# Kernel optimization log

Hardware: AMD Instinct MI355X
Metric: run time of the kernel (lower is better)

## Reference

```python
import math
import jax, jax.numpy as jnp
import numpy as np

D_MODEL = 1024
NUM_HEADS = 16
D_K = D_MODEL // NUM_HEADS
THETA = 10000.0
MAX_SEQ_LEN = 2048
BATCH = 2
SEQ = 2048


def build_rope_matrices(theta, d_k, max_seq_len):
    # Faithful to the torch buffer: per-position d_k x d_k tridiagonal rotation matrix.
    k = jnp.arange(d_k)
    inv_freq = jnp.power(theta, -2.0 * (k // 2) / d_k)  # [d_k]
    pos = jnp.arange(max_seq_len, dtype=jnp.float32)[:, None]  # [S,1]
    ang = pos * inv_freq[None, :]  # [S, d_k]
    cos_v = jnp.cos(ang)  # main diagonal
    sin_v = jnp.sin(jnp.where(k % 2 == 0, ang, 0.0))[:, :-1]  # sub/super diagonal, len d_k-1

    def mk(c, s):
        return jnp.diag(c) + jnp.diag(s, -1) + jnp.diag(-s, 1)

    return jax.vmap(mk)(cos_v, sin_v)  # [max_seq_len, d_k, d_k]


def setup_inputs() -> dict:
    key = jax.random.key(0)
    k1, k2, k3 = jax.random.split(key, 3)
    x = jax.random.normal(k1, (BATCH, SEQ, D_MODEL), dtype=jnp.float32)
    token_positions = jnp.arange(SEQ, dtype=jnp.int64 if jax.config.jax_enable_x64 else jnp.int32)
    # trunc_normal init approximated by scaled normal (same distribution family / scale)
    std_attn = 2.0 / (D_MODEL + 3 * D_MODEL)
    std_out = 2.0 / (D_MODEL + D_MODEL)
    W_attn = jax.random.normal(k2, (3 * NUM_HEADS * D_K, D_MODEL), dtype=jnp.float32) * std_attn
    W_out = jax.random.normal(k3, (D_MODEL, NUM_HEADS * D_K), dtype=jnp.float32) * std_out
    rope = build_rope_matrices(THETA, D_K, MAX_SEQ_LEN)
    return {"x": x, "W_attn": W_attn, "W_out": W_out, "rope": rope,
            "token_positions": token_positions}


def reference(x, W_attn, W_out, rope, token_positions):
    B, S, _ = x.shape
    # QKV projection: '... d_in, d_out d_in -> ... d_out'
    proj = jnp.einsum('bsd,ed->bse', x, W_attn)  # [B,S,3*H*dk]
    proj = proj.reshape(B, S, 3, NUM_HEADS, D_K)
    proj = jnp.transpose(proj, (2, 0, 3, 1, 4))  # [3,B,H,S,dk]
    Q, K, V = proj[0], proj[1], proj[2]
    # RoPE via per-position matrix multiply (faithful to module)
    R = rope[token_positions]  # [S, dk, dk]
    Q = jnp.einsum('sij,bhsj->bhsi', R, Q)
    K = jnp.einsum('sij,bhsj->bhsi', R, K)
    # naive causal attention with full score matrix (faithful)
    scores = jnp.einsum('bhnd,bhmd->bhnm', Q, K) / math.sqrt(D_K)
    causal = jnp.tril(jnp.ones((S, S), dtype=bool))
    scores = jnp.where(causal, scores, -jnp.inf)
    attn = jax.nn.softmax(scores, axis=-1)
    attended = jnp.einsum('bhnm,bhmd->bhnd', attn, V)  # [B,H,S,dk]
    concat = jnp.transpose(attended, (0, 2, 1, 3)).reshape(B, S, NUM_HEADS * D_K)
    return jnp.einsum('bse,de->bsd', concat, W_out)
```

## Files before the change

### kernel.cpp

```cpp
#include <hip/hip_runtime.h>
#include <math.h>

#define B_SZ 2
#define SEQ 2048
#define DMODEL 1024
#define NH 16
#define DK 64
#define NQKV 3072
#define M_ROWS 4096

#define NEG_BIG (-3.0e38f)
#define SCL 0.18033688011112042f

typedef short short8 __attribute__((ext_vector_type(8)));
typedef float v4f __attribute__((ext_vector_type(4)));
typedef unsigned short ushort_t;

__device__ inline ushort_t f2bf(float f) {
    unsigned u = __float_as_uint(f);
    u += 0x7fffu + ((u >> 16) & 1u);
    return (ushort_t)(u >> 16);
}

__device__ __forceinline__ void gl_lds16(const ushort_t* g, ushort_t* l) {
    __builtin_amdgcn_global_load_lds(
        (const __attribute__((address_space(1))) unsigned int*)g,
        (__attribute__((address_space(3))) unsigned int*)l, 16, 0, 0);
}

__global__ __launch_bounds__(256) void prep_kernel(
    const float* __restrict__ x, const float* __restrict__ Wa,
    const float* __restrict__ Wo, const float* __restrict__ rope,
    ushort_t* __restrict__ xb, ushort_t* __restrict__ Wab, ushort_t* __restrict__ Wob,
    float* __restrict__ cosT, float* __restrict__ sinT)
{
    const int bid = blockIdx.x;
    if (bid < 8192) {
        const float* src; ushort_t* dst; int i;
        if (bid < 4096)      { src = x;  dst = xb;  i = bid * 256 + threadIdx.x; }
        else if (bid < 7168) { src = Wa; dst = Wab; i = (bid - 4096) * 256 + threadIdx.x; }
        else                 { src = Wo; dst = Wob; i = (bid - 7168) * 256 + threadIdx.x; }
        float4 v = reinterpret_cast<const float4*>(src)[i];
        ushort4 r;
        r.x = f2bf(v.x); r.y = f2bf(v.y); r.z = f2bf(v.z); r.w = f2bf(v.w);
        reinterpret_cast<ushort4*>(dst)[i] = r;
    } else {
        const int i = (bid - 8192) * 256 + threadIdx.x;
        const int p = i >> 6, d = i & 63;
        const float* Rp = rope + (size_t)p * 4096;
        const float c = Rp[d * 64 + d];
        const float s = Rp[(d | 1) * 64 + (d & ~1)];
        cosT[i] = c;
        sinT[i] = (d & 1) ? s : -s;
    }
}

#define ES_STRIDE 136
extern __shared__ ushort_t qkv_smem[];

__global__ __launch_bounds__(256) void qkv_mfma_kernel(
    const ushort_t* __restrict__ xb,
    const ushort_t* __restrict__ Wab,
    const float* __restrict__ cosT, const float* __restrict__ sinT,
    const int* __restrict__ tpos,
    ushort_t* __restrict__ Qb, ushort_t* __restrict__ Kb, ushort_t* __restrict__ Vtb)
{
    ushort_t* Es = qkv_smem;

    const int tid = threadIdx.x;
    const int w = tid >> 6, lane = tid & 63;
    const int lm = lane & 15, g = lane >> 4;
    const int wm = (w >> 1) * 64, wn = (w & 1) * 64;
    const int e0 = blockIdx.x * 128, m0 = blockIdx.y * 128;

    int srow[8], skc[8];
#pragma unroll
    for (int j = 0; j < 8; ++j) {
        const int c = tid + 256 * j;
        const int cm = c & 1023;
        const int row = cm >> 3, pp = cm & 7;
        srow[j] = row;
        skc[j] = (pp ^ (row & 7)) * 8;
    }

    v4f acc[4][4] = {};

    for (int k0 = 0; k0 < DMODEL; k0 += 64) {
        __syncthreads();
#pragma unroll
        for (int j = 0; j < 4; ++j)
            gl_lds16(&Wab[(size_t)(e0 + srow[j]) * DMODEL + k0 + skc[j]],
                     &qkv_smem[(tid + 256 * j) * 8]);
#pragma unroll
        for (int j = 4; j < 8; ++j)
            gl_lds16(&xb [(size_t)(m0 + srow[j]) * DMODEL + k0 + skc[j]],
                     &qkv_smem[(tid + 256 * j) * 8]);
        __syncthreads();

#pragma unroll
        for (int kb = 0; kb < 2; ++kb) {
            short8 af[4], bfr[4];
#pragma unroll
            for (int mf = 0; mf < 4; ++mf) {
                const int r = wm + mf * 16 + lm;
                af[mf] = *reinterpret_cast<const short8*>(
                    &qkv_smem[(r * 8 + ((kb * 4 + g) ^ (r & 7))) * 8]);
            }
#pragma unroll
            for (int nf = 0; nf < 4; ++nf) {
                const int r = wn + nf * 16 + lm;
                bfr[nf] = *reinterpret_cast<const short8*>(
                    &qkv_smem[8192 + (r * 8 + ((kb * 4 + g) ^ (r & 7))) * 8]);
            }
#pragma unroll
            for (int mf = 0; mf < 4; ++mf)
#pragma unroll
                for (int nf = 0; nf < 4; ++nf)
                    acc[mf][nf] = __builtin_amdgcn_mfma_f32_16x16x32_bf16(af[mf], bfr[nf], acc[mf][nf], 0, 0, 0);
        }
    }

    __syncthreads();

    const int which = e0 >> 10;
    const int h0 = (e0 & 1023) >> 6;
    const int bb = m0 >> 11, s0 = m0 & 2047;

    if (which < 2) {
        ushort_t* buf = (which == 0) ? Qb : Kb;
#pragma unroll
        for (int mf = 0; mf < 4; ++mf) {
            const int ebase = wm + mf * 16 + g * 4;
            const int d0 = (e0 + ebase) & 63;
#pragma unroll
            for (int nf = 0; nf < 4; ++nf) {
                const int sloc = wn + nf * 16 + lm;
                float v[4] = {acc[mf][nf][0], acc[mf][nf][1], acc[mf][nf][2], acc[mf][nf][3]};
                const int p = tpos[s0 + sloc];
                const float4 c4 = *reinterpret_cast<const float4*>(&cosT[p * 64 + d0]);
                const float4 s4 = *reinterpret_cast<const float4*>(&sinT[p * 64 + d0]);
                const float r0 = c4.x * v[0] + s4.x * v[1];
                const float r1 = c4.y * v[1] + s4.y * v[0];
                const float r2 = c4.z * v[2] + s4.z * v[3];
                const float r3 = c4.w * v[3] + s4.w * v[2];
                uint2 pp;
                pp.x = (unsigned)f2bf(r0) | ((unsigned)f2bf(r1) << 16);
                pp.y = (unsigned)f2bf(r2) | ((unsigned)f2bf(r3) << 16);
                *reinterpret_cast<uint2*>(&Es[sloc * ES_STRIDE + ebase]) = pp;
            }
        }
        __syncthreads();
#pragma unroll
        for (int hh = 0; hh < 2; ++hh) {
            ushort_t* dst = buf + (((size_t)bb * NH + h0 + hh) * SEQ + s0) * DK;
#pragma unroll
            for (int t = 0; t < 4; ++t) {
                const int o = (t * 256 + tid) * 8;
                const int sloc = o >> 6, d = o & 63;
                const short8 vv = *reinterpret_cast<const short8*>(&Es[sloc * ES_STRIDE + hh * 64 + d]);
                *reinterpret_cast<short8*>(&dst[o]) = vv;
            }
        }
    } else {
#pragma unroll
        for (int mf = 0; mf < 4; ++mf) {
            const int ebase = wm + mf * 16 + g * 4;
#pragma unroll
            for (int nf = 0; nf < 4; ++nf) {
                const int sloc = wn + nf * 16 + lm;
                Es[(ebase + 0) * ES_STRIDE + sloc] = f2bf(acc[mf][nf][0]);
                Es[(ebase + 1) * ES_STRIDE + sloc] = f2bf(acc[mf][nf][1]);
                Es[(ebase + 2) * ES_STRIDE + sloc] = f2bf(acc[mf][nf][2]);
                Es[(ebase + 3) * ES_STRIDE + sloc] = f2bf(acc[mf][nf][3]);
            }
        }
        __syncthreads();
#pragma unroll
        for (int t = 0; t < 8; ++t) {
            const int c = t * 256 + tid;
            const int hh = c >> 10, cm = c & 1023;
            const int d = cm >> 4, s8c = (cm & 15) * 8;
            const short8 vv = *reinterpret_cast<const short8*>(&Es[(hh * 64 + d) * ES_STRIDE + s8c]);
            ushort_t* dst = Vtb + ((size_t)bb * NH + h0 + hh) * SEQ * DK + (size_t)d * SEQ + s0 + s8c;
            *reinterpret_cast<short8*>(dst) = vv;
        }
    }
}

#define ATTN_STEP(KSB, VSB, QF0, QF1, QROW, LSUM, OA, DIAG, C0)                   \
    {                                                                             \
        v4f sacc[4] = {};                                                         \
        _Pragma("unroll")                                                         \
        for (int nf = 0; nf < 4; ++nf) {                                          \
            const short8 kf0 = *reinterpret_cast<const short8*>(&KSB[nf * 16 + lm][lk8]);      \
            const short8 kf1 = *reinterpret_cast<const short8*>(&KSB[nf * 16 + lm][32 + lk8]); \
            sacc[nf] = __builtin_amdgcn_mfma_f32_16x16x32_bf16(kf0, QF0, sacc[nf], 0, 0, 0);   \
            sacc[nf] = __builtin_amdgcn_mfma_f32_16x16x32_bf16(kf1, QF1, sacc[nf], 0, 0, 0);   \
        }                                                                         \
        if (DIAG) {                                                               \
            _Pragma("unroll")                                                     \
            for (int nf = 0; nf < 4; ++nf)                                        \
                _Pragma("unroll")                                                 \
                for (int reg = 0; reg < 4; ++reg) {                               \
                    const int kv = (C0) + nf * 16 + g * 4 + reg;                  \
                    const float sv = sacc[nf][reg] * SCL;                         \
                    sacc[nf][reg] = (kv > (QROW)) ? NEG_BIG : sv;                 \
                }                                                                 \
        } else {                                                                  \
            _Pragma("unroll")                                                     \
            for (int nf = 0; nf < 4; ++nf)                                        \
                _Pragma("unroll")                                                 \
                for (int reg = 0; reg < 4; ++reg) sacc[nf][reg] *= SCL;           \
        }                                                                         \
        _Pragma("unroll")                                                         \
        for (int nf = 0; nf < 4; ++nf) {                                          \
            _Pragma("unroll")                                                     \
            for (int reg = 0; reg < 4; ++reg) {                                   \
                const float p = exp2f(sacc[nf][reg]);                             \
                sacc[nf][reg] = p;                                                \
                LSUM += p;                                                        \
            }                                                                     \
            uint2 pp;                                                             \
            pp.x = (unsigned)f2bf(sacc[nf][0]) | ((unsigned)f2bf(sacc[nf][1]) << 16); \
            pp.y = (unsigned)f2bf(sacc[nf][2]) | ((unsigned)f2bf(sacc[nf][3]) << 16); \
            *reinterpret_cast<uint2*>(&Ps[w * 16 + lm][nf * 16 + g * 4]) = pp;    \
        }                                                                         \
        _Pragma("unroll")                                                         \
        for (int kc = 0; kc < 2; ++kc) {                                          \
            const short8 pf = *reinterpret_cast<const short8*>(&Ps[w * 16 + lm][kc * 32 + lk8]); \
            _Pragma("unroll")                                                     \
            for (int df = 0; df < 4; ++df) {                                      \
                const short8 vf = *reinterpret_cast<const short8*>(&VSB[df * 16 + lm][kc * 32 + lk8]); \
                OA[df] = __builtin_amdgcn_mfma_f32_16x16x32_bf16(vf, pf, OA[df], 0, 0, 0); \
            }                                                                     \
        }                                                                         \
    }

__global__ __launch_bounds__(256) void attn_mfma_kernel(
    const ushort_t* __restrict__ Qb, const ushort_t* __restrict__ Kb,
    const ushort_t* __restrict__ Vtb, ushort_t* __restrict__ attb)
{
    __shared__ ushort_t Ks[2][64][72];
    __shared__ ushort_t Vs[2][64][72];
    __shared__ ushort_t Ps[64][72];

    const int tid = threadIdx.x;
    const int w = tid >> 6, lane = tid & 63;
    const int lm = lane & 15, g = lane >> 4, lk8 = g * 8;

    const int u = blockIdx.x;
    const int h = blockIdx.y, b = blockIdx.z;
    const size_t ho = ((size_t)b * NH + h) * SEQ * DK;
    const ushort_t* Qh = Qb + ho;
    const ushort_t* Kh = Kb + ho;
    const ushort_t* Vth = Vtb + ho;

    const int rr0 = tid >> 3, cc80 = (tid & 7) * 8;
    const int rr1 = (tid + 256) >> 3, cc81 = ((tid + 256) & 7) * 8;

    const int it1 = u, it2 = 31 - u;
    const int qrowA = it1 * 64 + w * 16 + lm;
    const int qrowB = it2 * 64 + w * 16 + lm;

    const short8 qa0 = *reinterpret_cast<const short8*>(&Qh[(size_t)qrowA * DK + lk8]);
    const short8 qa1 = *reinterpret_cast<const short8*>(&Qh[(size_t)qrowA * DK + 32 + lk8]);
    const short8 qb0 = *reinterpret_cast<const short8*>(&Qh[(size_t)qrowB * DK + lk8]);
    const short8 qb1 = *reinterpret_cast<const short8*>(&Qh[(size_t)qrowB * DK + 32 + lk8]);

    float lA = 0.f, lB = 0.f;
    v4f OA[4] = {}, OB[4] = {};

    short8 kreg[2], vreg[2];
    kreg[0] = *reinterpret_cast<const short8*>(&Kh[(size_t)rr0 * DK + cc80]);
    kreg[1] = *reinterpret_cast<const short8*>(&Kh[(size_t)rr1 * DK + cc81]);
    vreg[0] = *reinterpret_cast<const short8*>(&Vth[(size_t)rr0 * SEQ + cc80]);
    vreg[1] = *reinterpret_cast<const short8*>(&Vth[(size_t)rr1 * SEQ + cc81]);

    for (int jt = 0; jt <= it2; ++jt) {
        const int c0 = jt * 64;
        const int bufi = jt & 1;
        ushort_t (*Ksb)[72] = Ks[bufi];
        ushort_t (*Vsb)[72] = Vs[bufi];

        *reinterpret_cast<short8*>(&Ksb[rr0][cc80]) = kreg[0];
        *reinterpret_cast<short8*>(&Ksb[rr1][cc81]) = kreg[1];
        *reinterpret_cast<short8*>(&Vsb[rr0][cc80]) = vreg[0];
        *reinterpret_cast<short8*>(&Vsb[rr1][cc81]) = vreg[1];

        if (jt < it2) {
            const int c0n = c0 + 64;
            kreg[0] = *reinterpret_cast<const short8*>(&Kh[(size_t)(c0n + rr0) * DK + cc80]);
            kreg[1] = *reinterpret_cast<const short8*>(&Kh[(size_t)(c0n + rr1) * DK + cc81]);
            vreg[0] = *reinterpret_cast<const short8*>(&Vth[(size_t)rr0 * SEQ + c0n + cc80]);
            vreg[1] = *reinterpret_cast<const short8*>(&Vth[(size_t)rr1 * SEQ + c0n + cc81]);
        }

        __syncthreads();

        ATTN_STEP(Ksb, Vsb, qb0, qb1, qrowB, lB, OB, (jt == it2), c0)
        if (jt <= it1) {
            ATTN_STEP(Ksb, Vsb, qa0, qa1, qrowA, lA, OA, (jt == it1), c0)
        }
    }

    lA += __shfl_xor(lA, 16, 64); lA += __shfl_xor(lA, 32, 64);
    lB += __shfl_xor(lB, 16, 64); lB += __shfl_xor(lB, 32, 64);
    {
        const float inv = 1.0f / lA;
#pragma unroll
        for (int df = 0; df < 4; ++df) {
            const unsigned lo = (unsigned)f2bf(OA[df][0] * inv) | ((unsigned)f2bf(OA[df][1] * inv) << 16);
            const unsigned hi = (unsigned)f2bf(OA[df][2] * inv) | ((unsigned)f2bf(OA[df][3] * inv) << 16);
            uint2 st; st.x = lo; st.y = hi;
            *reinterpret_cast<uint2*>(
                &attb[((size_t)b * SEQ + qrowA) * DMODEL + h * DK + df * 16 + g * 4]) = st;
        }
    }
    {
        const float inv = 1.0f / lB;
#pragma unroll
        for (int df = 0; df < 4; ++df) {
            const unsigned lo = (unsigned)f2bf(OB[df][0] * inv) | ((unsigned)f2bf(OB[df][1] * inv) << 16);
            const unsigned hi = (unsigned)f2bf(OB[df][2] * inv) | ((unsigned)f2bf(OB[df][3] * inv) << 16);
            uint2 st; st.x = lo; st.y = hi;
            *reinterpret_cast<uint2*>(
                &attb[((size_t)b * SEQ + qrowB) * DMODEL + h * DK + df * 16 + g * 4]) = st;
        }
    }
}

__global__ __launch_bounds__(256) void out_mfma_kernel(
    const ushort_t* __restrict__ attb,
    const ushort_t* __restrict__ Wob,
    float* __restrict__ out)
{
    __shared__ ushort_t smem[16384];

    const int tid = threadIdx.x;
    const int w = tid >> 6, lane = tid & 63;
    const int lm = lane & 15, g = lane >> 4;
    const int wm = (w >> 1) * 64, wn = (w & 1) * 64;
    const int m0 = blockIdx.y * 128, n0 = blockIdx.x * 128;

    int srow[8], skc[8];
#pragma unroll
    for (int j = 0; j < 8; ++j) {
        const int c = tid + 256 * j;
        const int cm = c & 1023;
        const int row = cm >> 3, pp = cm & 7;
        srow[j] = row;
        skc[j] = (pp ^ (row & 7)) * 8;
    }

    v4f acc[4][4] = {};

    for (int k0 = 0; k0 < DMODEL; k0 += 64) {
        __syncthreads();
#pragma unroll
        for (int j = 0; j < 4; ++j)
            gl_lds16(&attb[(size_t)(m0 + srow[j]) * DMODEL + k0 + skc[j]],
                     &smem[(tid + 256 * j) * 8]);
#pragma unroll
        for (int j = 4; j < 8; ++j)
            gl_lds16(&Wob[(size_t)(n0 + srow[j]) * DMODEL + k0 + skc[j]],
                     &smem[(tid + 256 * j) * 8]);
        __syncthreads();

#pragma unroll
        for (int kb = 0; kb < 2; ++kb) {
            short8 af[4], bfr[4];
#pragma unroll
            for (int mf = 0; mf < 4; ++mf) {
                const int r = wm + mf * 16 + lm;
                af[mf] = *reinterpret_cast<const short8*>(
                    &smem[(r * 8 + ((kb * 4 + g) ^ (r & 7))) * 8]);
            }
#pragma unroll
            for (int nf = 0; nf < 4; ++nf) {
                const int r = wn + nf * 16 + lm;
                bfr[nf] = *reinterpret_cast<const short8*>(
                    &smem[8192 + (r * 8 + ((kb * 4 + g) ^ (r & 7))) * 8]);
            }
#pragma unroll
            for (int mf = 0; mf < 4; ++mf)
#pragma unroll
                for (int nf = 0; nf < 4; ++nf)
                    acc[mf][nf] = __builtin_amdgcn_mfma_f32_16x16x32_bf16(af[mf], bfr[nf], acc[mf][nf], 0, 0, 0);
        }
    }

#pragma unroll
    for (int mf = 0; mf < 4; ++mf)
#pragma unroll
        for (int reg = 0; reg < 4; ++reg) {
            const int m = m0 + wm + mf * 16 + g * 4 + reg;
#pragma unroll
            for (int nf = 0; nf < 4; ++nf) {
                const int n = n0 + wn + nf * 16 + lm;
                out[(size_t)m * DMODEL + n] = acc[mf][nf][reg];
            }
        }
}

extern "C" void kernel_launch(void* const* d_in, const int* in_sizes, int n_in,
                              void* d_out, int out_size, void* d_ws, size_t ws_size,
                              hipStream_t stream) {
    (void)in_sizes; (void)n_in; (void)out_size; (void)ws_size;

    const float* x    = (const float*)d_in[0];
    const float* Wa   = (const float*)d_in[1];
    const float* Wo   = (const float*)d_in[2];
    const float* rope = (const float*)d_in[3];
    const int*   tp   = (const int*)d_in[4];
    float* out = (float*)d_out;

    char* ws = (char*)d_ws;
    ushort_t* xb   = (ushort_t*)(ws);
    ushort_t* Wab  = (ushort_t*)(ws + (8u << 20));
    ushort_t* Wob  = (ushort_t*)(ws + (14u << 20));
    float*    cosT = (float*)   (ws + (16u << 20));
    float*    sinT = (float*)   (ws + (16u << 20) + (512u << 10));
    ushort_t* Qb   = (ushort_t*)(ws + (17u << 20));
    ushort_t* Kb   = (ushort_t*)(ws + (25u << 20));
    ushort_t* Vtb  = (ushort_t*)(ws + (33u << 20));
    ushort_t* attb = (ushort_t*)(ws + (41u << 20));

    dim3 blk(256);
    prep_kernel<<<dim3(8704), blk, 0, stream>>>(x, Wa, Wo, rope, xb, Wab, Wob, cosT, sinT);

    const size_t qkv_lds = 128 * ES_STRIDE * sizeof(ushort_t);
    qkv_mfma_kernel<<<dim3(NQKV / 128, M_ROWS / 128), blk, qkv_lds, stream>>>(
        xb, Wab, cosT, sinT, tp, Qb, Kb, Vtb);
    attn_mfma_kernel<<<dim3(16, NH, B_SZ), blk, 0, stream>>>(Qb, Kb, Vtb, attb);
    out_mfma_kernel<<<dim3(DMODEL / 128, M_ROWS / 128), blk, 0, stream>>>(attb, Wob, out);
}
```

Baseline: 225.9 us.

## Keep attention P in registers via permlane swaps and MFMA row sums

```diff
diff --git a/kernel.cpp b/kernel.cpp
--- a/kernel.cpp
+++ b/kernel.cpp
@@ -20,6 +20,18 @@
     unsigned u = __float_as_uint(f);
     u += 0x7fffu + ((u >> 16) & 1u);
     return (ushort_t)(u >> 16);
+}
+
+__device__ __forceinline__ unsigned cvt_pk_bf16(float lo, float hi) {
+    unsigned r;
+    asm("v_cvt_pk_bf16_f32 %0, %1, %2" : "=v"(r) : "v"(lo), "v"(hi));
+    return r;
+}
+__device__ __forceinline__ void permlane32_swap(unsigned &a, unsigned &b) {
+    asm("v_permlane32_swap_b32 %0, %1" : "+v"(a), "+v"(b));
+}
+__device__ __forceinline__ void permlane16_swap(unsigned &a, unsigned &b) {
+    asm("v_permlane16_swap_b32 %0, %1" : "+v"(a), "+v"(b));
 }
 
 __device__ __forceinline__ void gl_lds16(const ushort_t* g, ushort_t* l) {
@@ -128,6 +140,7 @@
 
     if (which < 2) {
         ushort_t* buf = (which == 0) ? Qb : Kb;
+        const float qs = (which == 0) ? SCL : 1.0f;
 #pragma unroll
         for (int mf = 0; mf < 4; ++mf) {
             const int ebase = wm + mf * 16 + g * 4;
@@ -139,10 +152,10 @@
                 const int p = tpos[s0 + sloc];
                 const float4 c4 = *reinterpret_cast<const float4*>(&cosT[p * 64 + d0]);
                 const float4 s4 = *reinterpret_cast<const float4*>(&sinT[p * 64 + d0]);
-                const float r0 = c4.x * v[0] + s4.x * v[1];
-                const float r1 = c4.y * v[1] + s4.y * v[0];
-                const float r2 = c4.z * v[2] + s4.z * v[3];
-                const float r3 = c4.w * v[3] + s4.w * v[2];
+                const float r0 = (c4.x * v[0] + s4.x * v[1]) * qs;
+                const float r1 = (c4.y * v[1] + s4.y * v[0]) * qs;
+                const float r2 = (c4.z * v[2] + s4.z * v[3]) * qs;
+                const float r3 = (c4.w * v[3] + s4.w * v[2]) * qs;
                 uint2 pp;
                 pp.x = (unsigned)f2bf(r0) | ((unsigned)f2bf(r1) << 16);
                 pp.y = (unsigned)f2bf(r2) | ((unsigned)f2bf(r3) << 16);
@@ -187,15 +200,13 @@
     }
 }
 
-#define ATTN_STEP(KSB, VSB, QF0, QF1, QROW, LSUM, OA, DIAG, C0)                   \
+#define ATTN_STEP(QF0, QF1, QROW, LACC, OACC, DIAG, C0)                           \
     {                                                                             \
         v4f sacc[4] = {};                                                         \
         _Pragma("unroll")                                                         \
         for (int nf = 0; nf < 4; ++nf) {                                          \
-            const short8 kf0 = *reinterpret_cast<const short8*>(&KSB[nf * 16 + lm][lk8]);      \
-            const short8 kf1 = *reinterpret_cast<const short8*>(&KSB[nf * 16 + lm][32 + lk8]); \
-            sacc[nf] = __builtin_amdgcn_mfma_f32_16x16x32_bf16(kf0, QF0, sacc[nf], 0, 0, 0);   \
-            sacc[nf] = __builtin_amdgcn_mfma_f32_16x16x32_bf16(kf1, QF1, sacc[nf], 0, 0, 0);   \
+            sacc[nf] = __builtin_amdgcn_mfma_f32_16x16x32_bf16(kf[nf][0], QF0, sacc[nf], 0, 0, 0); \
+            sacc[nf] = __builtin_amdgcn_mfma_f32_16x16x32_bf16(kf[nf][1], QF1, sacc[nf], 0, 0, 0); \
         }                                                                         \
         if (DIAG) {                                                               \
             _Pragma("unroll")                                                     \
@@ -203,46 +214,37 @@
                 _Pragma("unroll")                                                 \
                 for (int reg = 0; reg < 4; ++reg) {                               \
                     const int kv = (C0) + nf * 16 + g * 4 + reg;                  \
-                    const float sv = sacc[nf][reg] * SCL;                         \
-                    sacc[nf][reg] = (kv > (QROW)) ? NEG_BIG : sv;                 \
+                    if (kv > (QROW)) sacc[nf][reg] = NEG_BIG;                     \
                 }                                                                 \
-        } else {                                                                  \
-            _Pragma("unroll")                                                     \
-            for (int nf = 0; nf < 4; ++nf)                                        \
-                _Pragma("unroll")                                                 \
-                for (int reg = 0; reg < 4; ++reg) sacc[nf][reg] *= SCL;           \
         }                                                                         \
+        unsigned pk0[8];                                                          \
         _Pragma("unroll")                                                         \
         for (int nf = 0; nf < 4; ++nf) {                                          \
-            _Pragma("unroll")                                                     \
-            for (int reg = 0; reg < 4; ++reg) {                                   \
-                const float p = exp2f(sacc[nf][reg]);                             \
-                sacc[nf][reg] = p;                                                \
-                LSUM += p;                                                        \
-            }                                                                     \
-            uint2 pp;                                                             \
-            pp.x = (unsigned)f2bf(sacc[nf][0]) | ((unsigned)f2bf(sacc[nf][1]) << 16); \
-            pp.y = (unsigned)f2bf(sacc[nf][2]) | ((unsigned)f2bf(sacc[nf][3]) << 16); \
-            *reinterpret_cast<uint2*>(&Ps[w * 16 + lm][nf * 16 + g * 4]) = pp;    \
+            pk0[nf * 2]     = cvt_pk_bf16(exp2f(sacc[nf][0]), exp2f(sacc[nf][1])); \
+            pk0[nf * 2 + 1] = cvt_pk_bf16(exp2f(sacc[nf][2]), exp2f(sacc[nf][3])); \
         }                                                                         \
         _Pragma("unroll")                                                         \
         for (int kc = 0; kc < 2; ++kc) {                                          \
-            const short8 pf = *reinterpret_cast<const short8*>(&Ps[w * 16 + lm][kc * 32 + lk8]); \
+            unsigned x0 = pk0[kc * 4 + 0], y0 = pk0[kc * 4 + 2];                  \
+            unsigned x1 = pk0[kc * 4 + 1], y1 = pk0[kc * 4 + 3];                  \
+            permlane32_swap(x0, y0); permlane16_swap(x0, y0);                     \
+            permlane32_swap(x1, y1); permlane16_swap(x1, y1);                     \
+            union { unsigned u[4]; short8 s; } pu;                                \
+            pu.u[0] = x0; pu.u[1] = x1; pu.u[2] = y0; pu.u[3] = y1;               \
+            const short8 pf = pu.s;                                               \
+            LACC = __builtin_amdgcn_mfma_f32_16x16x32_bf16(ones8, pf, LACC, 0, 0, 0); \
             _Pragma("unroll")                                                     \
-            for (int df = 0; df < 4; ++df) {                                      \
-                const short8 vf = *reinterpret_cast<const short8*>(&VSB[df * 16 + lm][kc * 32 + lk8]); \
-                OA[df] = __builtin_amdgcn_mfma_f32_16x16x32_bf16(vf, pf, OA[df], 0, 0, 0); \
-            }                                                                     \
+            for (int df = 0; df < 4; ++df)                                        \
+                OACC[df] = __builtin_amdgcn_mfma_f32_16x16x32_bf16(vf[df][kc], pf, OACC[df], 0, 0, 0); \
         }                                                                         \
     }
 
-__global__ __launch_bounds__(256) void attn_mfma_kernel(
+__global__ __launch_bounds__(256, 2) void attn_mfma_kernel(
     const ushort_t* __restrict__ Qb, const ushort_t* __restrict__ Kb,
     const ushort_t* __restrict__ Vtb, ushort_t* __restrict__ attb)
 {
     __shared__ ushort_t Ks[2][64][72];
     __shared__ ushort_t Vs[2][64][72];
-    __shared__ ushort_t Ps[64][72];
 
     const int tid = threadIdx.x;
     const int w = tid >> 6, lane = tid & 63;
@@ -267,7 +269,9 @@
     const short8 qb0 = *reinterpret_cast<const short8*>(&Qh[(size_t)qrowB * DK + lk8]);
     const short8 qb1 = *reinterpret_cast<const short8*>(&Qh[(size_t)qrowB * DK + 32 + lk8]);
 
-    float lA = 0.f, lB = 0.f;
+    const short8 ones8 = {16256, 16256, 16256, 16256, 16256, 16256, 16256, 16256};
+
+    v4f laccA = {}, laccB = {};
     v4f OA[4] = {}, OB[4] = {};
 
     short8 kreg[2], vreg[2];
@@ -297,32 +301,42 @@
 
         __syncthreads();
 
-        ATTN_STEP(Ksb, Vsb, qb0, qb1, qrowB, lB, OB, (jt == it2), c0)
+        short8 kf[4][2], vf[4][2];
+#pragma unroll
+        for (int nf = 0; nf < 4; ++nf) {
+            kf[nf][0] = *reinterpret_cast<const short8*>(&Ksb[nf * 16 + lm][lk8]);
+            kf[nf][1] = *reinterpret_cast<const short8*>(&Ksb[nf * 16 + lm][32 + lk8]);
+        }
+#pragma unroll
+        for (int df = 0; df < 4; ++df) {
+            vf[df][0] = *reinterpret_cast<const short8*>(&Vsb[df * 16 + lm][lk8]);
+            vf[df][1] = *reinterpret_cast<const short8*>(&Vsb[df * 16 + lm][32 + lk8]);
+        }
+
+        ATTN_STEP(qb0, qb1, qrowB, laccB, OB, (jt == it2), c0)
         if (jt <= it1) {
-            ATTN_STEP(Ksb, Vsb, qa0, qa1, qrowA, lA, OA, (jt == it1), c0)
-        }
-    }
-
-    lA += __shfl_xor(lA, 16, 64); lA += __shfl_xor(lA, 32, 64);
-    lB += __shfl_xor(lB, 16, 64); lB += __shfl_xor(lB, 32, 64);
+            ATTN_STEP(qa0, qa1, qrowA, laccA, OA, (jt == it1), c0)
+        }
+    }
+
     {
-        const float inv = 1.0f / lA;
+        const float inv = 1.0f / laccA[0];
 #pragma unroll
         for (int df = 0; df < 4; ++df) {
-            const unsigned lo = (unsigned)f2bf(OA[df][0] * inv) | ((unsigned)f2bf(OA[df][1] * inv) << 16);
-            const unsigned hi = (unsigned)f2bf(OA[df][2] * inv) | ((unsigned)f2bf(OA[df][3] * inv) << 16);
-            uint2 st; st.x = lo; st.y = hi;
+            uint2 st;
+            st.x = cvt_pk_bf16(OA[df][0] * inv, OA[df][1] * inv);
+            st.y = cvt_pk_bf16(OA[df][2] * inv, OA[df][3] * inv);
             *reinterpret_cast<uint2*>(
                 &attb[((size_t)b * SEQ + qrowA) * DMODEL + h * DK + df * 16 + g * 4]) = st;
         }
     }
     {
-        const float inv = 1.0f / lB;
+        const float inv = 1.0f / laccB[0];
 #pragma unroll
         for (int df = 0; df < 4; ++df) {
-            const unsigned lo = (unsigned)f2bf(OB[df][0] * inv) | ((unsigned)f2bf(OB[df][1] * inv) << 16);
-            const unsigned hi = (unsigned)f2bf(OB[df][2] * inv) | ((unsigned)f2bf(OB[df][3] * inv) << 16);
-            uint2 st; st.x = lo; st.y = hi;
+            uint2 st;
+            st.x = cvt_pk_bf16(OB[df][0] * inv, OB[df][1] * inv);
+            st.y = cvt_pk_bf16(OB[df][2] * inv, OB[df][3] * inv);
             *reinterpret_cast<uint2*>(
                 &attb[((size_t)b * SEQ + qrowB) * DMODEL + h * DK + df * 16 + g * 4]) = st;
         }
```

Result: faster. 217.4 us (-3.8%).
